# Performance work log

Measured on AMD Instinct MI355X. Metric: run time of the kernel, lower is better.

The kernel has to match this reference:

```python
import jax, jax.numpy as jnp
import numpy as np

B, D, H, M, N, S = 256, 256, 512, 64, 2048, 3
SHIFTS = (1, 0, -1)  # = range(S//2, -S//2, -1); matches np.roll(eye, s, axis=1) one-hot matrices


def setup_inputs():
    key = jax.random.key(0)
    k = jax.random.split(key, 24)
    f32 = jnp.float32

    def rn(i, shape, scale):
        return jax.random.normal(k[i], shape, f32) * scale

    rh = jax.random.uniform(k[3], (B, N), f32)
    wh = jax.random.uniform(k[4], (B, N), f32)
    sc_ih = 1.0 / np.sqrt(D + M)
    sc_h = 1.0 / np.sqrt(H)
    return dict(
        inp=rn(0, (B, D), 1.0),
        h_tm1=rn(1, (B, H), 0.1),
        c_tm1=rn(2, (B, H), 0.1),
        read_head_tm1=rh / rh.sum(1, keepdims=True),
        write_head_tm1=wh / wh.sum(1, keepdims=True),
        memory=rn(5, (B, N, M), 0.5),
        W_ih=rn(6, (4 * H, D + M), sc_ih), W_hh=rn(7, (4 * H, H), sc_h),
        b_ih=jnp.zeros((4 * H,), f32), b_hh=jnp.zeros((4 * H,), f32),
        W_rk=rn(8, (M, H), sc_h), b_rk=rn(9, (M,), 0.01),
        W_wk=rn(10, (M, H), sc_h), b_wk=rn(11, (M,), 0.01),
        W_rc=rn(12, (3, H), sc_h), b_rc=jnp.zeros((3,), f32),
        W_wc=rn(13, (3, H), sc_h), b_wc=jnp.zeros((3,), f32),
        W_rs=rn(14, (S, H), sc_h), b_rs=jnp.zeros((S,), f32),
        W_ws=rn(15, (S, H), sc_h), b_ws=jnp.zeros((S,), f32),
        W_w=rn(16, (2 * M, H), sc_h), b_w=jnp.zeros((2 * M,), f32),
    )


def _head_params(h, Wk, bk, Wc, bc, Ws, bs):
    kk = jnp.tanh(h @ Wk.T + bk)                     # [B,M] key
    c = h @ Wc.T + bc                                # [B,3]
    beta = jax.nn.relu(c[:, 0:1]) + 1e-4             # focus strength
    g = jax.nn.sigmoid(c[:, 1:2])                    # interpolation gate
    gamma = jax.nn.relu(c[:, 2:3]) + 1.0001          # sharpening power
    s = jax.nn.softmax(h @ Ws.T + bs, axis=1)        # [B,S] shift weights
    return kk, s, beta, g, gamma


def _address(memory, head_tm1, kk, s, beta, g, gamma):
    dot = jnp.einsum('bm,bnm->bn', kk, memory)
    nk = jnp.linalg.norm(kk, axis=1, keepdims=True)  # [B,1]
    nM = jnp.linalg.norm(memory, axis=2)             # [B,N]
    cos = dot / jnp.maximum(nk * nM, 1e-8)
    content = jax.nn.softmax(beta * cos, axis=1)
    inter = g * content + (1.0 - g) * head_tm1       # gated interpolation [B,N]
    # circular shift; identical math to contracting with the one-hot C tensor
    rolled = jnp.stack([jnp.roll(inter, -sh, axis=1) for sh in SHIFTS], axis=1)  # [B,S,N]
    out = jnp.einsum('bsn,bs->bn', rolled, s)
    out = out ** gamma                               # sharpen
    return out / out.sum(1, keepdims=True)


def reference(inp, h_tm1, c_tm1, read_head_tm1, write_head_tm1, memory,
              W_ih, W_hh, b_ih, b_hh, W_rk, b_rk, W_wk, b_wk,
              W_rc, b_rc, W_wc, b_wc, W_rs, b_rs, W_ws, b_ws, W_w, b_w):
    # read addressing uses previous hidden state
    rp = _head_params(h_tm1, W_rk, b_rk, W_rc, b_rc, W_rs, b_rs)
    read_head = _address(memory, read_head_tm1, *rp)
    M_read = jnp.einsum('bn,bnm->bm', read_head, memory)  # [B,M]
    # LSTMCell controller (torch gate order i,f,g,o)
    x = jnp.concatenate([inp, M_read], axis=1)
    z = x @ W_ih.T + b_ih + h_tm1 @ W_hh.T + b_hh
    zi, zf, zg, zo = jnp.split(z, 4, axis=1)
    c_t = jax.nn.sigmoid(zf) * c_tm1 + jax.nn.sigmoid(zi) * jnp.tanh(zg)
    h_t = jax.nn.sigmoid(zo) * jnp.tanh(c_t)
    # write addressing uses new hidden state
    wp = _head_params(h_t, W_wk, b_wk, W_wc, b_wc, W_ws, b_ws)
    write_head = _address(memory, write_head_tm1, *wp)
    wa = h_t @ W_w.T + b_w
    e = jax.nn.sigmoid(wa[:, :M])                    # erase
    a = jnp.tanh(wa[:, M:])                          # add
    ww = write_head[:, :, None]                      # [B,N,1]
    M_out = memory * (1.0 - ww * e[:, None, :]) + ww * a[:, None, :]
    return (h_t, c_t, read_head, write_head, M_out)
```

## Files before the change

kernel.cpp:

```cpp
#include <hip/hip_runtime.h>
#include <hip/hip_bf16.h>

#define Bb 256
#define Hh 512
#define Mm 64
#define Nn 2048

typedef __attribute__((ext_vector_type(8))) short bf16x8;
typedef __attribute__((ext_vector_type(4))) float f32x4;
typedef __attribute__((ext_vector_type(4))) unsigned short u16x4;

static __device__ __forceinline__ short f2bf(float f) {
    unsigned u = __float_as_uint(f);
    unsigned r = (u + 0x7FFFu + ((u >> 16) & 1u)) >> 16;
    return (short)r;
}
static __device__ __forceinline__ float bf2f(unsigned short u) {
    return __uint_as_float(((unsigned)u) << 16);
}

__global__ __launch_bounds__(256) void convW_headparams_kernel(
    const float* __restrict__ W_ih, const float* __restrict__ W_hh,
    short* __restrict__ Wb,
    const float* __restrict__ h,
    const float* __restrict__ Wk, const float* __restrict__ bk,
    const float* __restrict__ Wc, const float* __restrict__ bc,
    const float* __restrict__ Ws, const float* __restrict__ bs,
    float* __restrict__ kk, float* __restrict__ par)
{
    if (blockIdx.x < 832) {
        unsigned g = blockIdx.x * 256 + threadIdx.x;
        unsigned j = g / 104u;
        unsigned kq = (g - j * 104u) * 8u;
        const float* src = (kq < 320u) ? (W_ih + (size_t)j * 320 + kq)
                                       : (W_hh + (size_t)j * 512 + (kq - 320u));
        float4 a = ((const float4*)src)[0];
        float4 c = ((const float4*)src)[1];
        bf16x8 o;
        o[0] = f2bf(a.x); o[1] = f2bf(a.y); o[2] = f2bf(a.z); o[3] = f2bf(a.w);
        o[4] = f2bf(c.x); o[5] = f2bf(c.y); o[6] = f2bf(c.z); o[7] = f2bf(c.w);
        *(bf16x8*)(Wb + (size_t)j * 832 + kq) = o;
        return;
    }
    int b = blockIdx.x - 832;
    __shared__ float hs[Hh];
    __shared__ float red[6];
    __shared__ float skk[Mm];
    const float* hb = h + (size_t)b * Hh;
    for (int i = threadIdx.x; i < Hh; i += 256) hs[i] = hb[i];
    __syncthreads();
    int m = threadIdx.x >> 2, sub = threadIdx.x & 3;
    {
        const float* w = Wk + (size_t)m * Hh + sub * 128;
        const float* hh = hs + sub * 128;
        float acc = 0.f;
        #pragma unroll 8
        for (int k = 0; k < 128; ++k) acc += hh[k] * w[k];
        acc += __shfl_xor(acc, 1, 64);
        acc += __shfl_xor(acc, 2, 64);
        if (sub == 0) {
            float v = tanhf(acc + bk[m]);
            kk[(size_t)b * Mm + m] = v;
            skk[m] = v;
        }
    }
    if (threadIdx.x < 24) {
        int o = threadIdx.x >> 2, su = threadIdx.x & 3;
        const float* w = ((o < 3) ? (Wc + (size_t)o * Hh) : (Ws + (size_t)(o - 3) * Hh)) + su * 128;
        const float* hh = hs + su * 128;
        float acc = 0.f;
        #pragma unroll 8
        for (int k = 0; k < 128; ++k) acc += hh[k] * w[k];
        acc += __shfl_xor(acc, 1, 64);
        acc += __shfl_xor(acc, 2, 64);
        if (su == 0) red[o] = acc + ((o < 3) ? bc[o] : bs[o - 3]);
    }
    __syncthreads();
    if (threadIdx.x == 0) {
        float beta  = fmaxf(red[0], 0.f) + 1e-4f;
        float g     = 1.f / (1.f + __expf(-red[1]));
        float gamma = fmaxf(red[2], 0.f) + 1.0001f;
        float l0 = red[3], l1 = red[4], l2 = red[5];
        float mx = fmaxf(l0, fmaxf(l1, l2));
        float e0 = __expf(l0 - mx), e1 = __expf(l1 - mx), e2 = __expf(l2 - mx);
        float inv = 1.f / (e0 + e1 + e2);
        float ssq = 0.f;
        #pragma unroll
        for (int i = 0; i < Mm; ++i) ssq += skk[i] * skk[i];
        float* p = par + (size_t)b * 8;
        p[0] = beta; p[1] = g; p[2] = gamma;
        p[3] = e0 * inv; p[4] = e1 * inv; p[5] = e2 * inv;
        p[6] = sqrtf(ssq);
    }
}

__global__ __launch_bounds__(256) void convM_cos_kernel(
    const float* __restrict__ mem, const float* __restrict__ kk,
    const float* __restrict__ par, float* __restrict__ cosv,
    short* __restrict__ memb)
{
    int b  = blockIdx.x >> 3;
    int n0 = (blockIdx.x & 7) << 8;
    int w  = threadIdx.x >> 6;
    int l  = threadIdx.x & 63;
    int m4 = l & 15;
    int rq = l >> 4;

    float4 kv = ((const float4*)(kk + (size_t)b * Mm))[m4];
    float kn = par[(size_t)b * 8 + 6];
    const float4* mb4 = (const float4*)(mem + (size_t)b * Nn * Mm);
    short* ob = memb + (size_t)b * Nn * Mm;

    #pragma unroll
    for (int q = 0; q < 16; ++q) {
        int n = n0 + w * 64 + q * 4 + rq;
        float4 v = mb4[(size_t)n * 16 + m4];
        u16x4 o;
        o[0] = (unsigned short)f2bf(v.x); o[1] = (unsigned short)f2bf(v.y);
        o[2] = (unsigned short)f2bf(v.z); o[3] = (unsigned short)f2bf(v.w);
        *(u16x4*)(ob + (size_t)n * 64 + m4 * 4) = o;
        float dot = v.x * kv.x + v.y * kv.y + v.z * kv.z + v.w * kv.w;
        float ss  = v.x * v.x + v.y * v.y + v.z * v.z + v.w * v.w;
        dot += __shfl_xor(dot, 1, 64); ss += __shfl_xor(ss, 1, 64);
        dot += __shfl_xor(dot, 2, 64); ss += __shfl_xor(ss, 2, 64);
        dot += __shfl_xor(dot, 4, 64); ss += __shfl_xor(ss, 4, 64);
        dot += __shfl_xor(dot, 8, 64); ss += __shfl_xor(ss, 8, 64);
        if (m4 == 0) cosv[(size_t)b * Nn + n] = dot / fmaxf(kn * sqrtf(ss), 1e-8f);
    }
}

__global__ __launch_bounds__(1024) void raddr_mread_convA_kernel(
    const float* __restrict__ cosv, const float* __restrict__ par,
    const float* __restrict__ prev, const short* __restrict__ memb,
    const float* __restrict__ inp, const float* __restrict__ h,
    float* __restrict__ outh, short* __restrict__ Ab)
{
    int b = blockIdx.x;
    int t = threadIdx.x;
    int w = t >> 6, l = t & 63;
    __shared__ float csh[Nn];
    __shared__ float redw[16];
    __shared__ float4 red4[64][16];
    __shared__ float mrdL[Mm];

    const float* pv = par + (size_t)b * 8;
    float beta = pv[0], g = pv[1], gamma = pv[2];
    float s0 = pv[3], s1 = pv[4], s2 = pv[5];

    float v0 = beta * cosv[(size_t)b * Nn + t];
    float v1 = beta * cosv[(size_t)b * Nn + t + 1024];
    float mx = fmaxf(v0, v1);
    #pragma unroll
    for (int msk = 1; msk < 64; msk <<= 1) mx = fmaxf(mx, __shfl_xor(mx, msk, 64));
    if (l == 0) redw[w] = mx;
    __syncthreads();
    mx = redw[0];
    #pragma unroll
    for (int i = 1; i < 16; ++i) mx = fmaxf(mx, redw[i]);
    float e0 = __expf(v0 - mx), e1 = __expf(v1 - mx);
    float sum = e0 + e1;
    #pragma unroll
    for (int msk = 1; msk < 64; msk <<= 1) sum += __shfl_xor(sum, msk, 64);
    __syncthreads();
    if (l == 0) redw[w] = sum;
    __syncthreads();
    sum = 0.f;
    #pragma unroll
    for (int i = 0; i < 16; ++i) sum += redw[i];
    float invs = 1.f / sum;
    const float* pb = prev + (size_t)b * Nn;
    float i0 = g * e0 * invs + (1.f - g) * pb[t];
    float i1 = g * e1 * invs + (1.f - g) * pb[t + 1024];
    csh[t] = i0; csh[t + 1024] = i1;
    __syncthreads();
    int n1 = t + 1024;
    float c0 = s0 * csh[(t + 1) & (Nn - 1)] + s1 * i0 + s2 * csh[(t - 1) & (Nn - 1)];
    float c1 = s0 * csh[(n1 + 1) & (Nn - 1)] + s1 * i1 + s2 * csh[(n1 - 1) & (Nn - 1)];
    float p0 = exp2f(gamma * __log2f(c0));
    float p1 = exp2f(gamma * __log2f(c1));
    float osum = p0 + p1;
    #pragma unroll
    for (int msk = 1; msk < 64; msk <<= 1) osum += __shfl_xor(osum, msk, 64);
    __syncthreads();
    if (l == 0) redw[w] = osum;
    __syncthreads();
    osum = 0.f;
    #pragma unroll
    for (int i = 0; i < 16; ++i) osum += redw[i];
    float inv2 = 1.f / osum;
    float h0 = p0 * inv2, h1 = p1 * inv2;
    outh[(size_t)b * Nn + t] = h0;
    outh[(size_t)b * Nn + n1] = h1;
    __syncthreads();
    csh[t] = h0; csh[n1] = h1;
    __syncthreads();

    int r = t >> 4;
    int c = t & 15;
    const short* mb = memb + (size_t)b * Nn * Mm;
    float ax = 0.f, ay = 0.f, az = 0.f, aw = 0.f;
    for (int n = r; n < Nn; n += 64) {
        float wgt = csh[n];
        u16x4 uv = *(const u16x4*)(mb + (size_t)n * 64 + c * 4);
        ax += wgt * bf2f(uv[0]); ay += wgt * bf2f(uv[1]);
        az += wgt * bf2f(uv[2]); aw += wgt * bf2f(uv[3]);
    }
    red4[r][c] = make_float4(ax, ay, az, aw);
    __syncthreads();
    if (t < 256) {
        int gg = t >> 4, cc = t & 15;
        float4 a = red4[gg * 4 + 0][cc], bq = red4[gg * 4 + 1][cc];
        float4 cv = red4[gg * 4 + 2][cc], d = red4[gg * 4 + 3][cc];
        red4[gg * 4][cc] = make_float4(a.x + bq.x + cv.x + d.x, a.y + bq.y + cv.y + d.y,
                                       a.z + bq.z + cv.z + d.z, a.w + bq.w + cv.w + d.w);
    }
    __syncthreads();
    if (t < 16) {
        float sx = 0.f, sy = 0.f, sz = 0.f, sw = 0.f;
        #pragma unroll
        for (int gg = 0; gg < 16; ++gg) {
            float4 v = red4[gg * 4][t];
            sx += v.x; sy += v.y; sz += v.z; sw += v.w;
        }
        mrdL[t * 4 + 0] = sx; mrdL[t * 4 + 1] = sy;
        mrdL[t * 4 + 2] = sz; mrdL[t * 4 + 3] = sw;
    }
    __syncthreads();

    if (t < 104) {
        int kq = t * 8;
        float v[8];
        if (kq < 256) {
            const float* s = inp + (size_t)b * 256 + kq;
            #pragma unroll
            for (int i = 0; i < 8; ++i) v[i] = s[i];
        } else if (kq < 320) {
            #pragma unroll
            for (int i = 0; i < 8; ++i) v[i] = mrdL[kq - 256 + i];
        } else {
            const float* s = h + (size_t)b * 512 + (kq - 320);
            #pragma unroll
            for (int i = 0; i < 8; ++i) v[i] = s[i];
        }
        bf16x8 o;
        #pragma unroll
        for (int i = 0; i < 8; ++i) o[i] = f2bf(v[i]);
        *(bf16x8*)(Ab + (size_t)b * 832 + kq) = o;
    }
}

#define LDA 56
__global__ __launch_bounds__(256) void lstm_gemm_mfma(
    const short* __restrict__ Ab, const short* __restrict__ Wb,
    const float* __restrict__ b_ih, const float* __restrict__ b_hh,
    float* __restrict__ z)
{
    __shared__ short As[64][LDA];
    __shared__ short Bs[64][LDA];
    int t = threadIdx.x;
    int r0 = blockIdx.x * 64, c0 = blockIdx.y * 64;
    int w = t >> 6, l = t & 63;
    int wr = (w >> 1) * 32, wc = (w & 1) * 32;
    int ar = t >> 2, kq = (t & 3) * 8;
    int lr = l & 15, kb = (l >> 4) * 8;

    f32x4 acc00 = {0.f, 0.f, 0.f, 0.f}, acc01 = {0.f, 0.f, 0.f, 0.f};
    f32x4 acc10 = {0.f, 0.f, 0.f, 0.f}, acc11 = {0.f, 0.f, 0.f, 0.f};

    for (int kt = 0; kt < 26; ++kt) {
        int k0 = kt * 32;
        *(bf16x8*)&As[ar][kq] = *(const bf16x8*)(Ab + (size_t)(r0 + ar) * 832 + k0 + kq);
        *(bf16x8*)&Bs[ar][kq] = *(const bf16x8*)(Wb + (size_t)(c0 + ar) * 832 + k0 + kq);
        __syncthreads();
        bf16x8 a0 = *(const bf16x8*)&As[wr + lr][kb];
        bf16x8 a1 = *(const bf16x8*)&As[wr + 16 + lr][kb];
        bf16x8 b0 = *(const bf16x8*)&Bs[wc + lr][kb];
        bf16x8 b1 = *(const bf16x8*)&Bs[wc + 16 + lr][kb];
        acc00 = __builtin_amdgcn_mfma_f32_16x16x32_bf16(a0, b0, acc00, 0, 0, 0);
        acc01 = __builtin_amdgcn_mfma_f32_16x16x32_bf16(a0, b1, acc01, 0, 0, 0);
        acc10 = __builtin_amdgcn_mfma_f32_16x16x32_bf16(a1, b0, acc10, 0, 0, 0);
        acc11 = __builtin_amdgcn_mfma_f32_16x16x32_bf16(a1, b1, acc11, 0, 0, 0);
        __syncthreads();
    }
    int rq = (l >> 4) * 4;
    #pragma unroll
    for (int q = 0; q < 4; ++q) {
        int row0 = r0 + wr + rq + q;
        int col0 = c0 + wc + lr;
        z[(size_t)row0 * 2048 + col0] = acc00[q] + b_ih[col0] + b_hh[col0];
        z[(size_t)row0 * 2048 + col0 + 16] = acc01[q] + b_ih[col0 + 16] + b_hh[col0 + 16];
        z[(size_t)(row0 + 16) * 2048 + col0] = acc10[q] + b_ih[col0] + b_hh[col0];
        z[(size_t)(row0 + 16) * 2048 + col0 + 16] = acc11[q] + b_ih[col0 + 16] + b_hh[col0 + 16];
    }
}

__global__ __launch_bounds__(1024) void gates_wparams_kernel(
    const float* __restrict__ z, const float* __restrict__ c_tm1,
    const float* __restrict__ Wk, const float* __restrict__ bk,
    const float* __restrict__ Wc, const float* __restrict__ bc,
    const float* __restrict__ Ws, const float* __restrict__ bs,
    const float* __restrict__ W_w, const float* __restrict__ b_w,
    float* __restrict__ h_out, float* __restrict__ c_out,
    float* __restrict__ kk, float* __restrict__ par, float* __restrict__ ea)
{
    int b = blockIdx.x;
    int t = threadIdx.x;
    __shared__ float hs[Hh];
    __shared__ float red6[6];
    __shared__ float skk[Mm];

    if (t < 512) {
        const float* zb = z + (size_t)b * 2048;
        float zi = zb[t], zf = zb[512 + t], zg = zb[1024 + t], zo = zb[1536 + t];
        float si = 1.f / (1.f + __expf(-zi));
        float sf = 1.f / (1.f + __expf(-zf));
        float so = 1.f / (1.f + __expf(-zo));
        float ct = sf * c_tm1[(size_t)b * 512 + t] + si * tanhf(zg);
        float ht = so * tanhf(ct);
        c_out[(size_t)b * 512 + t] = ct;
        h_out[(size_t)b * 512 + t] = ht;
        hs[t] = ht;
    }
    __syncthreads();

    if (t < 256) {
        int m = t >> 2, sub = t & 3;
        const float* w = Wk + (size_t)m * Hh + sub * 128;
        const float* hh = hs + sub * 128;
        float acc = 0.f;
        #pragma unroll 8
        for (int k = 0; k < 128; ++k) acc += hh[k] * w[k];
        acc += __shfl_xor(acc, 1, 64);
        acc += __shfl_xor(acc, 2, 64);
        if (sub == 0) {
            float v = tanhf(acc + bk[m]);
            skk[m] = v;
            kk[(size_t)b * Mm + m] = v;
        }
    } else if (t < 280) {
        int o = (t - 256) >> 2, su = t & 3;
        const float* w = ((o < 3) ? (Wc + (size_t)o * Hh) : (Ws + (size_t)(o - 3) * Hh)) + su * 128;
        const float* hh = hs + su * 128;
        float acc = 0.f;
        #pragma unroll 8
        for (int k = 0; k < 128; ++k) acc += hh[k] * w[k];
        acc += __shfl_xor(acc, 1, 64);
        acc += __shfl_xor(acc, 2, 64);
        if (su == 0) red6[o] = acc + ((o < 3) ? bc[o] : bs[o - 3]);
    } else if (t >= 512) {
        int o = (t - 512) >> 2, su = t & 3;
        const float* w = W_w + (size_t)o * Hh + su * 128;
        const float* hh = hs + su * 128;
        float acc = 0.f;
        #pragma unroll 8
        for (int k = 0; k < 128; ++k) acc += hh[k] * w[k];
        acc += __shfl_xor(acc, 1, 64);
        acc += __shfl_xor(acc, 2, 64);
        if (su == 0) {
            float v = acc + b_w[o];
            ea[(size_t)b * 128 + o] = (o < Mm) ? (1.f / (1.f + __expf(-v))) : tanhf(v);
        }
    }
    __syncthreads();
    if (t < 64) {
        float v = skk[t];
        float ssq = v * v;
        #pragma unroll
        for (int msk = 1; msk < 64; msk <<= 1) ssq += __shfl_xor(ssq, msk, 64);
        if (t == 0) {
            float beta  = fmaxf(red6[0], 0.f) + 1e-4f;
            float g     = 1.f / (1.f + __expf(-red6[1]));
            float gamma = fmaxf(red6[2], 0.f) + 1.0001f;
            float l0 = red6[3], l1 = red6[4], l2 = red6[5];
            float mx = fmaxf(l0, fmaxf(l1, l2));
            float e0 = __expf(l0 - mx), e1 = __expf(l1 - mx), e2 = __expf(l2 - mx);
            float inv = 1.f / (e0 + e1 + e2);
            float* p = par + (size_t)b * 8;
            p[0] = beta; p[1] = g; p[2] = gamma;
            p[3] = e0 * inv; p[4] = e1 * inv; p[5] = e2 * inv;
            p[6] = sqrtf(ssq);
        }
    }
}

__global__ __launch_bounds__(1024) void wfused_kernel(
    const short* __restrict__ memb, const float* __restrict__ kk,
    const float* __restrict__ par, const float* __restrict__ prev,
    float* __restrict__ outh)
{
    int b = blockIdx.x;
    int t = threadIdx.x;
    int w = t >> 6, l = t & 63;
    int m4 = l & 15, rq = l >> 4;
    __shared__ float csh[Nn];
    __shared__ float redw[16];

    const float* pv = par + (size_t)b * 8;
    float kn = pv[6];
    float beta = pv[0], g = pv[1], gamma = pv[2];
    float s0 = pv[3], s1 = pv[4], s2 = pv[5];
    float4 kv = ((const float4*)(kk + (size_t)b * Mm))[m4];
    const short* mb = memb + (size_t)b * Nn * Mm;

    #pragma unroll 4
    for (int it = 0; it < 32; ++it) {
        int n = it * 64 + w * 4 + rq;
        u16x4 uv = *(const u16x4*)(mb + (size_t)n * 64 + m4 * 4);
        float x0 = bf2f(uv[0]), x1 = bf2f(uv[1]), x2 = bf2f(uv[2]), x3 = bf2f(uv[3]);
        float dot = x0 * kv.x + x1 * kv.y + x2 * kv.z + x3 * kv.w;
        float ss  = x0 * x0 + x1 * x1 + x2 * x2 + x3 * x3;
        dot += __shfl_xor(dot, 1, 64); ss += __shfl_xor(ss, 1, 64);
        dot += __shfl_xor(dot, 2, 64); ss += __shfl_xor(ss, 2, 64);
        dot += __shfl_xor(dot, 4, 64); ss += __shfl_xor(ss, 4, 64);
        dot += __shfl_xor(dot, 8, 64); ss += __shfl_xor(ss, 8, 64);
        if (m4 == 0) csh[n] = dot / fmaxf(kn * sqrtf(ss), 1e-8f);
    }
    __syncthreads();

    float v0 = beta * csh[t], v1 = beta * csh[t + 1024];
    float mx = fmaxf(v0, v1);
    #pragma unroll
    for (int msk = 1; msk < 64; msk <<= 1) mx = fmaxf(mx, __shfl_xor(mx, msk, 64));
    if (l == 0) redw[w] = mx;
    __syncthreads();
    mx = redw[0];
    #pragma unroll
    for (int i = 1; i < 16; ++i) mx = fmaxf(mx, redw[i]);
    float e0 = __expf(v0 - mx), e1 = __expf(v1 - mx);
    float sum = e0 + e1;
    #pragma unroll
    for (int msk = 1; msk < 64; msk <<= 1) sum += __shfl_xor(sum, msk, 64);
    __syncthreads();
    if (l == 0) redw[w] = sum;
    __syncthreads();
    sum = 0.f;
    #pragma unroll
    for (int i = 0; i < 16; ++i) sum += redw[i];
    float invs = 1.f / sum;
    const float* pb = prev + (size_t)b * Nn;
    float i0 = g * e0 * invs + (1.f - g) * pb[t];
    float i1 = g * e1 * invs + (1.f - g) * pb[t + 1024];
    __syncthreads();
    csh[t] = i0; csh[t + 1024] = i1;
    __syncthreads();
    int n1 = t + 1024;
    float c0 = s0 * csh[(t + 1) & (Nn - 1)] + s1 * i0 + s2 * csh[(t - 1) & (Nn - 1)];
    float c1 = s0 * csh[(n1 + 1) & (Nn - 1)] + s1 * i1 + s2 * csh[(n1 - 1) & (Nn - 1)];
    float p0 = exp2f(gamma * __log2f(c0));
    float p1 = exp2f(gamma * __log2f(c1));
    float osum = p0 + p1;
    #pragma unroll
    for (int msk = 1; msk < 64; msk <<= 1) osum += __shfl_xor(osum, msk, 64);
    __syncthreads();
    if (l == 0) redw[w] = osum;
    __syncthreads();
    osum = 0.f;
    #pragma unroll
    for (int i = 0; i < 16; ++i) osum += redw[i];
    float inv2 = 1.f / osum;
    outh[(size_t)b * Nn + t] = p0 * inv2;
    outh[(size_t)b * Nn + n1] = p1 * inv2;
}

template <int BF16SRC>
__global__ __launch_bounds__(256) void mout_kernel(
    const float* __restrict__ mem, const short* __restrict__ memb,
    const float* __restrict__ head, const float* __restrict__ ea,
    float* __restrict__ out)
{
    const size_t total = (size_t)Bb * Nn * Mm / 4;
    for (size_t i4 = (size_t)blockIdx.x * 256 + threadIdx.x; i4 < total;
         i4 += (size_t)2048 * 256) {
        size_t row = i4 >> 4;
        int m4 = (int)(i4 & 15);
        int b = (int)(row >> 11);
        float w = head[row];
        float4 mv;
        if (BF16SRC) {
            u16x4 uv = ((const u16x4*)memb)[i4];
            mv = make_float4(bf2f(uv[0]), bf2f(uv[1]), bf2f(uv[2]), bf2f(uv[3]));
        } else {
            mv = ((const float4*)mem)[i4];
        }
        const float4* e4p = (const float4*)(ea + (size_t)b * 128);
        float4 ev = e4p[m4];
        float4 av = e4p[16 + m4];
        float4 o;
        o.x = mv.x * (1.f - w * ev.x) + w * av.x;
        o.y = mv.y * (1.f - w * ev.y) + w * av.y;
        o.z = mv.z * (1.f - w * ev.z) + w * av.z;
        o.w = mv.w * (1.f - w * ev.w) + w * av.w;
        ((float4*)out)[i4] = o;
    }
}

extern "C" void kernel_launch(void* const* d_in, const int* in_sizes, int n_in,
                              void* d_out, int out_size, void* d_ws, size_t ws_size,
                              hipStream_t stream)
{
    const float* inp   = (const float*)d_in[0];
    const float* h_tm1 = (const float*)d_in[1];
    const float* c_tm1 = (const float*)d_in[2];
    const float* rh0   = (const float*)d_in[3];
    const float* wh0   = (const float*)d_in[4];
    const float* mem   = (const float*)d_in[5];
    const float* W_ih  = (const float*)d_in[6];
    const float* W_hh  = (const float*)d_in[7];
    const float* b_ih  = (const float*)d_in[8];
    const float* b_hh  = (const float*)d_in[9];
    const float* W_rk  = (const float*)d_in[10];
    const float* b_rk  = (const float*)d_in[11];
    const float* W_wk  = (const float*)d_in[12];
    const float* b_wk  = (const float*)d_in[13];
    const float* W_rc  = (const float*)d_in[14];
    const float* b_rc  = (const float*)d_in[15];
    const float* W_wc  = (const float*)d_in[16];
    const float* b_wc  = (const float*)d_in[17];
    const float* W_rs  = (const float*)d_in[18];
    const float* b_rs  = (const float*)d_in[19];
    const float* W_ws  = (const float*)d_in[20];
    const float* b_ws  = (const float*)d_in[21];
    const float* W_w   = (const float*)d_in[22];
    const float* b_w   = (const float*)d_in[23];

    float* out   = (float*)d_out;
    float* h_t   = out;
    float* c_t   = out + 131072;
    float* rhead = out + 262144;
    float* whead = out + 786432;
    float* mo    = out + 1310720;
    float* cosbuf = mo;
    float* zbuf   = mo + 524288;
    short* Ab     = (short*)(mo + 1048576);
    short* Wb     = (short*)(mo + 1179648);

    float* ws  = (float*)d_ws;
    float* kk  = ws;
    float* par = ws + 16384;
    float* ea  = ws + 18432;

    const size_t memb_elems = (size_t)Bb * Nn * Mm;
    const bool big_ws = ws_size >= (size_t)51200 * 4 + memb_elems * 2;
    short* memb = big_ws ? (short*)(ws + 51200)
                         : (short*)(mo + 2097152);

    convW_headparams_kernel<<<1088, 256, 0, stream>>>(
        W_ih, W_hh, Wb, h_tm1, W_rk, b_rk, W_rc, b_rc, W_rs, b_rs, kk, par);
    convM_cos_kernel<<<2048, 256, 0, stream>>>(mem, kk, par, cosbuf, memb);
    raddr_mread_convA_kernel<<<Bb, 1024, 0, stream>>>(
        cosbuf, par, rh0, memb, inp, h_tm1, rhead, Ab);
    lstm_gemm_mfma<<<dim3(4, 32), 256, 0, stream>>>(Ab, Wb, b_ih, b_hh, zbuf);
    gates_wparams_kernel<<<Bb, 1024, 0, stream>>>(
        zbuf, c_tm1, W_wk, b_wk, W_wc, b_wc, W_ws, b_ws, W_w, b_w,
        h_t, c_t, kk, par, ea);
    wfused_kernel<<<Bb, 1024, 0, stream>>>(memb, kk, par, wh0, whead);
    if (big_ws)
        mout_kernel<1><<<2048, 256, 0, stream>>>(mem, memb, whead, ea, mo);
    else
        mout_kernel<0><<<2048, 256, 0, stream>>>(mem, memb, whead, ea, mo);
}
```

Baseline: 163.5 us.

## Widen bf16 memory accesses, add nontemporal hints, drop LDS staging in LSTM GEMM

Several unrelated tweaks land together. Nontemporal loads and stores are added on the streaming fp32 memory read in the convert kernel and in the output update kernel. The M_read and write-cosine passes switch to 16-byte bf16 loads with 8 elements per lane, and the M_read reduction becomes a shared-memory tree. The LSTM MFMA GEMM now loads operands straight from global memory instead of staging them through LDS with barriers. These changes aim to cut memory-instruction count, barriers and cache pollution, at the risk of uncoalesced direct global loads in the GEMM and a longer reduction tree.

```diff
diff --git a/kernel.cpp b/kernel.cpp
--- a/kernel.cpp
+++ b/kernel.cpp
@@ -9,6 +9,7 @@
 typedef __attribute__((ext_vector_type(8))) short bf16x8;
 typedef __attribute__((ext_vector_type(4))) float f32x4;
 typedef __attribute__((ext_vector_type(4))) unsigned short u16x4;
+typedef __attribute__((ext_vector_type(8))) unsigned short u16x8;
 
 static __device__ __forceinline__ short f2bf(float f) {
     unsigned u = __float_as_uint(f);
@@ -108,19 +109,19 @@
 
     float4 kv = ((const float4*)(kk + (size_t)b * Mm))[m4];
     float kn = par[(size_t)b * 8 + 6];
-    const float4* mb4 = (const float4*)(mem + (size_t)b * Nn * Mm);
+    const f32x4* mb4 = (const f32x4*)(mem + (size_t)b * Nn * Mm);
     short* ob = memb + (size_t)b * Nn * Mm;
 
     #pragma unroll
     for (int q = 0; q < 16; ++q) {
         int n = n0 + w * 64 + q * 4 + rq;
-        float4 v = mb4[(size_t)n * 16 + m4];
+        f32x4 v = __builtin_nontemporal_load(mb4 + (size_t)n * 16 + m4);
         u16x4 o;
-        o[0] = (unsigned short)f2bf(v.x); o[1] = (unsigned short)f2bf(v.y);
-        o[2] = (unsigned short)f2bf(v.z); o[3] = (unsigned short)f2bf(v.w);
+        o[0] = (unsigned short)f2bf(v[0]); o[1] = (unsigned short)f2bf(v[1]);
+        o[2] = (unsigned short)f2bf(v[2]); o[3] = (unsigned short)f2bf(v[3]);
         *(u16x4*)(ob + (size_t)n * 64 + m4 * 4) = o;
-        float dot = v.x * kv.x + v.y * kv.y + v.z * kv.z + v.w * kv.w;
-        float ss  = v.x * v.x + v.y * v.y + v.z * v.z + v.w * v.w;
+        float dot = v[0] * kv.x + v[1] * kv.y + v[2] * kv.z + v[3] * kv.w;
+        float ss  = v[0] * v[0] + v[1] * v[1] + v[2] * v[2] + v[3] * v[3];
         dot += __shfl_xor(dot, 1, 64); ss += __shfl_xor(ss, 1, 64);
         dot += __shfl_xor(dot, 2, 64); ss += __shfl_xor(ss, 2, 64);
         dot += __shfl_xor(dot, 4, 64); ss += __shfl_xor(ss, 4, 64);
@@ -140,7 +141,7 @@
     int w = t >> 6, l = t & 63;
     __shared__ float csh[Nn];
     __shared__ float redw[16];
-    __shared__ float4 red4[64][16];
+    __shared__ float redM[128][8][8];
     __shared__ float mrdL[Mm];
 
     const float* pv = par + (size_t)b * 8;
@@ -195,35 +196,32 @@
     csh[t] = h0; csh[n1] = h1;
     __syncthreads();
 
-    int r = t >> 4;
-    int c = t & 15;
+    int m8 = t & 7;
+    int r  = t >> 3;
     const short* mb = memb + (size_t)b * Nn * Mm;
-    float ax = 0.f, ay = 0.f, az = 0.f, aw = 0.f;
-    for (int n = r; n < Nn; n += 64) {
+    float acc[8] = {};
+    #pragma unroll 4
+    for (int it = 0; it < 16; ++it) {
+        int n = it * 128 + r;
         float wgt = csh[n];
-        u16x4 uv = *(const u16x4*)(mb + (size_t)n * 64 + c * 4);
-        ax += wgt * bf2f(uv[0]); ay += wgt * bf2f(uv[1]);
-        az += wgt * bf2f(uv[2]); aw += wgt * bf2f(uv[3]);
-    }
-    red4[r][c] = make_float4(ax, ay, az, aw);
-    __syncthreads();
-    if (t < 256) {
-        int gg = t >> 4, cc = t & 15;
-        float4 a = red4[gg * 4 + 0][cc], bq = red4[gg * 4 + 1][cc];
-        float4 cv = red4[gg * 4 + 2][cc], d = red4[gg * 4 + 3][cc];
-        red4[gg * 4][cc] = make_float4(a.x + bq.x + cv.x + d.x, a.y + bq.y + cv.y + d.y,
-                                       a.z + bq.z + cv.z + d.z, a.w + bq.w + cv.w + d.w);
-    }
-    __syncthreads();
-    if (t < 16) {
-        float sx = 0.f, sy = 0.f, sz = 0.f, sw = 0.f;
-        #pragma unroll
-        for (int gg = 0; gg < 16; ++gg) {
-            float4 v = red4[gg * 4][t];
-            sx += v.x; sy += v.y; sz += v.z; sw += v.w;
-        }
-        mrdL[t * 4 + 0] = sx; mrdL[t * 4 + 1] = sy;
-        mrdL[t * 4 + 2] = sz; mrdL[t * 4 + 3] = sw;
+        u16x8 uv = *(const u16x8*)(mb + (size_t)n * 64 + m8 * 8);
+        #pragma unroll
+        for (int j = 0; j < 8; ++j) acc[j] += wgt * bf2f(uv[j]);
+    }
+    #pragma unroll
+    for (int j = 0; j < 8; ++j) redM[r][m8][j] = acc[j];
+    __syncthreads();
+    #pragma unroll
+    for (int s = 64; s >= 1; s >>= 1) {
+        if (r < s) {
+            #pragma unroll
+            for (int j = 0; j < 8; ++j) redM[r][m8][j] += redM[r + s][m8][j];
+        }
+        __syncthreads();
+    }
+    if (t < 8) {
+        #pragma unroll
+        for (int j = 0; j < 8; ++j) mrdL[t * 8 + j] = redM[0][t][j];
     }
     __syncthreads();
 
@@ -249,38 +247,36 @@
     }
 }
 
-#define LDA 56
 __global__ __launch_bounds__(256) void lstm_gemm_mfma(
     const short* __restrict__ Ab, const short* __restrict__ Wb,
     const float* __restrict__ b_ih, const float* __restrict__ b_hh,
     float* __restrict__ z)
 {
-    __shared__ short As[64][LDA];
-    __shared__ short Bs[64][LDA];
     int t = threadIdx.x;
     int r0 = blockIdx.x * 64, c0 = blockIdx.y * 64;
     int w = t >> 6, l = t & 63;
     int wr = (w >> 1) * 32, wc = (w & 1) * 32;
-    int ar = t >> 2, kq = (t & 3) * 8;
     int lr = l & 15, kb = (l >> 4) * 8;
+
+    const short* A0 = Ab + (size_t)(r0 + wr + lr) * 832 + kb;
+    const short* A1 = A0 + 16 * 832;
+    const short* B0 = Wb + (size_t)(c0 + wc + lr) * 832 + kb;
+    const short* B1 = B0 + 16 * 832;
 
     f32x4 acc00 = {0.f, 0.f, 0.f, 0.f}, acc01 = {0.f, 0.f, 0.f, 0.f};
     f32x4 acc10 = {0.f, 0.f, 0.f, 0.f}, acc11 = {0.f, 0.f, 0.f, 0.f};
 
+    #pragma unroll 2
     for (int kt = 0; kt < 26; ++kt) {
         int k0 = kt * 32;
-        *(bf16x8*)&As[ar][kq] = *(const bf16x8*)(Ab + (size_t)(r0 + ar) * 832 + k0 + kq);
-        *(bf16x8*)&Bs[ar][kq] = *(const bf16x8*)(Wb + (size_t)(c0 + ar) * 832 + k0 + kq);
-        __syncthreads();
-        bf16x8 a0 = *(const bf16x8*)&As[wr + lr][kb];
-        bf16x8 a1 = *(const bf16x8*)&As[wr + 16 + lr][kb];
-        bf16x8 b0 = *(const bf16x8*)&Bs[wc + lr][kb];
-        bf16x8 b1 = *(const bf16x8*)&Bs[wc + 16 + lr][kb];
+        bf16x8 a0 = *(const bf16x8*)(A0 + k0);
+        bf16x8 a1 = *(const bf16x8*)(A1 + k0);
+        bf16x8 b0 = *(const bf16x8*)(B0 + k0);
+        bf16x8 b1 = *(const bf16x8*)(B1 + k0);
         acc00 = __builtin_amdgcn_mfma_f32_16x16x32_bf16(a0, b0, acc00, 0, 0, 0);
         acc01 = __builtin_amdgcn_mfma_f32_16x16x32_bf16(a0, b1, acc01, 0, 0, 0);
         acc10 = __builtin_amdgcn_mfma_f32_16x16x32_bf16(a1, b0, acc10, 0, 0, 0);
         acc11 = __builtin_amdgcn_mfma_f32_16x16x32_bf16(a1, b1, acc11, 0, 0, 0);
-        __syncthreads();
     }
     int rq = (l >> 4) * 4;
     #pragma unroll
@@ -391,7 +387,6 @@
     int b = blockIdx.x;
     int t = threadIdx.x;
     int w = t >> 6, l = t & 63;
-    int m4 = l & 15, rq = l >> 4;
     __shared__ float csh[Nn];
     __shared__ float redw[16];
 
@@ -399,21 +394,30 @@
     float kn = pv[6];
     float beta = pv[0], g = pv[1], gamma = pv[2];
     float s0 = pv[3], s1 = pv[4], s2 = pv[5];
-    float4 kv = ((const float4*)(kk + (size_t)b * Mm))[m4];
+
+    int m8 = l & 7, rg = l >> 3;
+    float kv[8];
+    {
+        const float* kp = kk + (size_t)b * Mm + m8 * 8;
+        #pragma unroll
+        for (int j = 0; j < 8; ++j) kv[j] = kp[j];
+    }
     const short* mb = memb + (size_t)b * Nn * Mm;
-
     #pragma unroll 4
-    for (int it = 0; it < 32; ++it) {
-        int n = it * 64 + w * 4 + rq;
-        u16x4 uv = *(const u16x4*)(mb + (size_t)n * 64 + m4 * 4);
-        float x0 = bf2f(uv[0]), x1 = bf2f(uv[1]), x2 = bf2f(uv[2]), x3 = bf2f(uv[3]);
-        float dot = x0 * kv.x + x1 * kv.y + x2 * kv.z + x3 * kv.w;
-        float ss  = x0 * x0 + x1 * x1 + x2 * x2 + x3 * x3;
+    for (int it = 0; it < 16; ++it) {
+        int n = it * 128 + w * 8 + rg;
+        u16x8 uv = *(const u16x8*)(mb + (size_t)n * 64 + m8 * 8);
+        float dot = 0.f, ss = 0.f;
+        #pragma unroll
+        for (int j = 0; j < 8; ++j) {
+            float x = bf2f(uv[j]);
+            dot += x * kv[j];
+            ss  += x * x;
+        }
         dot += __shfl_xor(dot, 1, 64); ss += __shfl_xor(ss, 1, 64);
         dot += __shfl_xor(dot, 2, 64); ss += __shfl_xor(ss, 2, 64);
         dot += __shfl_xor(dot, 4, 64); ss += __shfl_xor(ss, 4, 64);
-        dot += __shfl_xor(dot, 8, 64); ss += __shfl_xor(ss, 8, 64);
-        if (m4 == 0) csh[n] = dot / fmaxf(kn * sqrtf(ss), 1e-8f);
+        if (m8 == 0) csh[n] = dot / fmaxf(kn * sqrtf(ss), 1e-8f);
     }
     __syncthreads();
 
@@ -468,29 +472,34 @@
     const float* __restrict__ head, const float* __restrict__ ea,
     float* __restrict__ out)
 {
-    const size_t total = (size_t)Bb * Nn * Mm / 4;
-    for (size_t i4 = (size_t)blockIdx.x * 256 + threadIdx.x; i4 < total;
-         i4 += (size_t)2048 * 256) {
-        size_t row = i4 >> 4;
-        int m4 = (int)(i4 & 15);
+    const size_t total8 = (size_t)Bb * Nn * Mm / 8;
+    for (size_t i8 = (size_t)blockIdx.x * 256 + threadIdx.x; i8 < total8;
+         i8 += (size_t)2048 * 256) {
+        size_t row = i8 >> 3;
+        int m8 = (int)(i8 & 7);
         int b = (int)(row >> 11);
         float w = head[row];
-        float4 mv;
+        float x[8];
         if (BF16SRC) {
-            u16x4 uv = ((const u16x4*)memb)[i4];
-            mv = make_float4(bf2f(uv[0]), bf2f(uv[1]), bf2f(uv[2]), bf2f(uv[3]));
+            u16x8 uv = __builtin_nontemporal_load((const u16x8*)memb + i8);
+            #pragma unroll
+            for (int j = 0; j < 8; ++j) x[j] = bf2f(uv[j]);
         } else {
-            mv = ((const float4*)mem)[i4];
-        }
-        const float4* e4p = (const float4*)(ea + (size_t)b * 128);
-        float4 ev = e4p[m4];
-        float4 av = e4p[16 + m4];
-        float4 o;
-        o.x = mv.x * (1.f - w * ev.x) + w * av.x;
-        o.y = mv.y * (1.f - w * ev.y) + w * av.y;
-        o.z = mv.z * (1.f - w * ev.z) + w * av.z;
-        o.w = mv.w * (1.f - w * ev.w) + w * av.w;
-        ((float4*)out)[i4] = o;
+            f32x4 lo = __builtin_nontemporal_load((const f32x4*)mem + i8 * 2);
+            f32x4 hi = __builtin_nontemporal_load((const f32x4*)mem + i8 * 2 + 1);
+            #pragma unroll
+            for (int j = 0; j < 4; ++j) { x[j] = lo[j]; x[4 + j] = hi[j]; }
+        }
+        const float* ep = ea + (size_t)b * 128 + m8 * 8;
+        const float* ap = ep + 64;
+        f32x4 o0, o1;
+        #pragma unroll
+        for (int j = 0; j < 4; ++j) {
+            o0[j] = x[j] * (1.f - w * ep[j]) + w * ap[j];
+            o1[j] = x[4 + j] * (1.f - w * ep[4 + j]) + w * ap[4 + j];
+        }
+        __builtin_nontemporal_store(o0, (f32x4*)out + i8 * 2);
+        __builtin_nontemporal_store(o1, (f32x4*)out + i8 * 2 + 1);
     }
 }
 
```

Measured after the change: 155.6 us. 1.05x faster.
